# Optimization experiments

Hardware: AMD Instinct MI355X
Metric: run time of the kernel (lower is better)

## Reference

```python
import jax, jax.numpy as jnp
import numpy as np
from math import sqrt

B, NQ, SK, ISIZE, HSIZE, OSIZE, H = 4, 2048, 2048, 1024, 1024, 1024, 16
D = HSIZE // H  # attn_dim = 64
IEPS = 1e-32
NEG = -1e32

def setup_inputs() -> dict:
    key = jax.random.key(0)
    ks = jax.random.split(key, 9)
    scale = 1.0 / sqrt(ISIZE)
    return {
        "iQ": jax.random.normal(ks[0], (B, NQ, ISIZE), jnp.float32),
        "iK": jax.random.normal(ks[1], (B, SK, ISIZE), jnp.float32),
        "iV": jax.random.normal(ks[2], (B, SK, ISIZE), jnp.float32),
        "mask": jax.random.randint(ks[3], (B, NQ, SK), 0, 2).astype(bool),
        # torch nn.Linear weights: [out_features, in_features]
        "Wq": jax.random.normal(ks[4], (HSIZE, ISIZE), jnp.float32) * scale,
        "Wk": jax.random.normal(ks[5], (HSIZE, ISIZE), jnp.float32) * scale,
        "Wv": jax.random.normal(ks[6], (HSIZE, ISIZE), jnp.float32) * scale,
        "Wo": jax.random.normal(ks[7], (OSIZE, HSIZE), jnp.float32) * scale,
        "sn_bias": jnp.zeros((1,), jnp.float32),  # SparseNormer bias
    }

def reference(iQ, iK, iV, mask, Wq, Wk, Wv, Wo, sn_bias):
    b, nq, _ = iQ.shape
    sk = iK.shape[1]
    # projections, split into heads: [b, h, n, d]
    q = (iQ @ Wq.T).reshape(b, nq, H, D).transpose(0, 2, 1, 3)
    k = (iK @ Wk.T).reshape(b, sk, H, D).transpose(0, 2, 1, 3)
    v = (iV @ Wv.T).reshape(b, sk, H, D).transpose(0, 2, 1, 3)
    # scaled dot-product scores: [b, h, nq, sk]
    scores = jnp.einsum("bhqd,bhkd->bhqk", q, k) / sqrt(D)
    scores = jnp.where(mask[:, None, :, :], NEG, scores)
    # SparseNormer: relu(x + bias)^2 normalized along last dim
    t = jax.nn.relu(scores + sn_bias)
    t = t * t
    attn = t / (t.sum(-1, keepdims=True) + IEPS)
    o = jnp.einsum("bhqk,bhkd->bhqd", attn, v)
    o = o.transpose(0, 2, 1, 3).reshape(b, nq, HSIZE)
    return o @ Wo.T
```

## Files before the change

### kernel.cpp

```cpp
#include <hip/hip_runtime.h>
#include <stdint.h>

#define B_   4
#define NQ_  2048
#define SK_  2048
#define H_   16
#define HS_  1024
#define D_   64
#define TOKc ((size_t)B_ * NQ_ * HS_)
#define WEc  ((size_t)HS_ * HS_)

typedef __attribute__((ext_vector_type(8))) short bf16x8;
typedef __attribute__((ext_vector_type(4))) float f32x4;
typedef __attribute__((ext_vector_type(2))) float f32x2;
typedef __attribute__((ext_vector_type(8))) unsigned short u16x8;
typedef __attribute__((ext_vector_type(4))) int i32x4;

#define DEVI __device__ __forceinline__

DEVI unsigned short f2bf_hu(float f) {
  union { float f; unsigned int i; } x; x.f = f;
  return (unsigned short)((x.i + 0x8000u) >> 16);
}
DEVI unsigned int pack2(float a, float b) {
  union { float f; unsigned int i; } x, y; x.f = a; y.f = b;
  return __builtin_amdgcn_perm(y.i + 0x8000u, x.i + 0x8000u, 0x07060302u);
}
DEVI u16x8 cvt8(f32x4 lo, f32x4 hi) {
  union { u16x8 s; unsigned int w[4]; } r;
  r.w[0] = pack2(lo[0], lo[1]);
  r.w[1] = pack2(lo[2], lo[3]);
  r.w[2] = pack2(hi[0], hi[1]);
  r.w[3] = pack2(hi[2], hi[3]);
  return r.s;
}
DEVI void async16(void* lds, const void* g) {
  __builtin_amdgcn_global_load_lds(
      (const __attribute__((address_space(1))) unsigned int*)g,
      (__attribute__((address_space(3))) unsigned int*)lds, 16, 0, 0);
}

DEVI f32x2 pkfma(f32x2 a, f32x2 b, f32x2 c) {
  f32x2 d;
  asm("v_pk_fma_f32 %0, %1, %2, %3" : "=v"(d) : "v"(a), "v"(b), "v"(c));
  return d;
}
DEVI f32x2 pkmul(f32x2 a, f32x2 b) {
  f32x2 d;
  asm("v_pk_mul_f32 %0, %1, %2" : "=v"(d) : "v"(a), "v"(b));
  return d;
}
DEVI f32x2 pkadd(f32x2 a, f32x2 b) {
  f32x2 d;
  asm("v_pk_add_f32 %0, %1, %2" : "=v"(d) : "v"(a), "v"(b));
  return d;
}
DEVI unsigned int cvtpk_bf16(float lo, float hi) {
  unsigned int r;
  asm("v_cvt_pk_bf16_f32 %0, %1, %2" : "=v"(r) : "v"(lo), "v"(hi));
  return r;
}
template <int OFF>
DEVI float keepf(float x, unsigned int nb) {
  int k;
  asm("v_bfe_i32 %0, %1, %2, 1" : "=v"(k) : "v"(nb), "i"(OFF));
  union { float f; int i; } u; u.f = x; u.i &= k;
  return u.f;
}

#define SWZB(row, colb) ((((row) * 128) + (colb)) ^ (((row) & 7) << 4))

__global__ __launch_bounds__(256)
void cvt_prep(const float* __restrict__ a, unsigned short* __restrict__ ab,
              const float* __restrict__ wsrc, unsigned short* __restrict__ wdst,
              int naBlocks) {
  const int bi = blockIdx.x;
  const float* s; unsigned short* d; size_t base;
  if (bi < naBlocks) { s = a;    d = ab;   base = (size_t)bi * 2048; }
  else               { s = wsrc; d = wdst; base = (size_t)(bi - naBlocks) * 2048; }
  const size_t o = base + (size_t)threadIdx.x * 8;
  f32x4 lo = *(const f32x4*)(s + o);
  f32x4 hi = *(const f32x4*)(s + o + 4);
  *(u16x8*)(d + o) = cvt8(lo, hi);
}

__global__ __launch_bounds__(256)
void cvt_all(const float* __restrict__ iQ, const float* __restrict__ iK,
             const float* __restrict__ iV, const float* __restrict__ Wq,
             const float* __restrict__ Wk, const float* __restrict__ Wv,
             const float* __restrict__ Wo, unsigned short* __restrict__ ACT,
             unsigned short* __restrict__ WALL) {
  const int bi = blockIdx.x;
  const float* s; unsigned short* d; size_t base;
  if (bi < 12288) {
    const int which = bi >> 12;
    s = (which == 0) ? iQ : (which == 1) ? iK : iV;
    d = ACT + (size_t)which * TOKc;
    base = (size_t)(bi & 4095) * 2048;
  } else {
    const int wi = (bi - 12288) >> 9;
    s = (wi == 0) ? Wq : (wi == 1) ? Wk : (wi == 2) ? Wv : Wo;
    d = WALL + (size_t)wi * WEc;
    base = (size_t)((bi - 12288) & 511) * 2048;
  }
  const size_t o = base + (size_t)threadIdx.x * 8;
  f32x4 lo = *(const f32x4*)(s + o);
  f32x4 hi = *(const f32x4*)(s + o + 4);
  *(u16x8*)(d + o) = cvt8(lo, hi);
}

__global__ __launch_bounds__(256)
void pack_mask(const int* __restrict__ m, unsigned long long* __restrict__ bits) {
  const size_t tid = (size_t)blockIdx.x * 256 + threadIdx.x;
  const unsigned long long bal = __ballot(m[tid] != 0);
  if ((threadIdx.x & 63) == 0) bits[tid >> 6] = bal;
}

template <bool CF32>
DEVI void gemm_body_pipe(const unsigned short* __restrict__ A,
                         const unsigned short* __restrict__ Wb,
                         void* __restrict__ Cp, int M, int N, int K,
                         unsigned short* As, unsigned short* Bs) {
  const int t = threadIdx.x;
  const int w = t >> 6, l = t & 63;
  const int lm = l & 15, lg = l >> 4;
  const int bm = blockIdx.x * 128, bn = blockIdx.y * 128;
  const int wm = (w >> 1) * 64, wn = (w & 1) * 64;

  const int sr = t >> 2;
  const int sg = ((t & 3) ^ ((t >> 3) & 3)) * 8;
  const unsigned short* Ag0 = A + (size_t)(bm + sr) * K + sg;
  const unsigned short* Ag1 = A + (size_t)(bm + sr + 64) * K + sg;
  const unsigned short* Wg0 = Wb + (size_t)(bn + sr) * K + sg;
  const unsigned short* Wg1 = Wb + (size_t)(bn + sr + 64) * K + sg;

  const int fx = (lm >> 1) & 3;
  f32x4 acc[4][4] = {};

  auto stage = [&](int bi, int k0) {
    unsigned short* la = As + bi * 4096 + t * 8;
    unsigned short* lb = Bs + bi * 4096 + t * 8;
    async16(la,        Ag0 + k0);
    async16(la + 2048, Ag1 + k0);
    async16(lb,        Wg0 + k0);
    async16(lb + 2048, Wg1 + k0);
  };

  stage(0, 0);
  int cur = 0;
  for (int k0 = 0; k0 < K; k0 += 32) {
    if (k0 + 32 < K) {
      stage(cur ^ 1, k0 + 32);
      asm volatile("s_waitcnt vmcnt(4)" ::: "memory");
    } else {
      asm volatile("s_waitcnt vmcnt(0)" ::: "memory");
    }
    __builtin_amdgcn_sched_barrier(0);
    __builtin_amdgcn_s_barrier();
    const unsigned short* Ab = As + cur * 4096;
    const unsigned short* Bb = Bs + cur * 4096;
    bf16x8 aF[4], bF[4];
#pragma unroll
    for (int i = 0; i < 4; i++)
      aF[i] = *(const bf16x8*)&Ab[(wm + i * 16 + lm) * 32 + ((lg ^ fx) * 8)];
#pragma unroll
    for (int i = 0; i < 4; i++)
      bF[i] = *(const bf16x8*)&Bb[(wn + i * 16 + lm) * 32 + ((lg ^ fx) * 8)];
    __builtin_amdgcn_s_setprio(1);
#pragma unroll
    for (int i = 0; i < 4; i++)
#pragma unroll
      for (int j = 0; j < 4; j++)
        acc[i][j] = __builtin_amdgcn_mfma_f32_16x16x32_bf16(aF[i], bF[j], acc[i][j], 0, 0, 0);
    __builtin_amdgcn_s_setprio(0);
    __builtin_amdgcn_s_barrier();
    cur ^= 1;
  }
#pragma unroll
  for (int i = 0; i < 4; i++)
#pragma unroll
    for (int j = 0; j < 4; j++) {
      const int row = bm + wm + i * 16 + lg * 4;
      const int col = bn + wn + j * 16 + lm;
#pragma unroll
      for (int r = 0; r < 4; r++) {
        if constexpr (CF32) {
          ((float*)Cp)[(size_t)(row + r) * N + col] = acc[i][j][r];
        } else {
          ((unsigned short*)Cp)[(size_t)(row + r) * N + col] = f2bf_hu(acc[i][j][r]);
        }
      }
    }
}

template <bool CF32>
__global__ __launch_bounds__(256)
void gemm_bb(const unsigned short* __restrict__ A, const unsigned short* __restrict__ Wb,
             void* __restrict__ Cp, int M, int N, int K) {
  __shared__ unsigned short As[2 * 128 * 32];
  __shared__ unsigned short Bs[2 * 128 * 32];
  gemm_body_pipe<CF32>(A, Wb, Cp, M, N, K, As, Bs);
}

__global__ __launch_bounds__(256)
void gemm_qkv(const unsigned short* __restrict__ ACT, const unsigned short* __restrict__ WALL,
              unsigned short* __restrict__ Qb, unsigned short* __restrict__ Kb,
              unsigned short* __restrict__ Vb, int M, int N, int K) {
  __shared__ unsigned short As[2 * 128 * 32];
  __shared__ unsigned short Bs[2 * 128 * 32];
  const int z = blockIdx.z;
  const unsigned short* A = ACT + (size_t)z * (size_t)M * (size_t)K;
  const unsigned short* W = WALL + (size_t)z * (size_t)N * (size_t)K;
  unsigned short* C = (z == 0) ? Qb : ((z == 1) ? Kb : Vb);
  gemm_body_pipe<false>(A, W, (void*)C, M, N, K, As, Bs);
}

template <bool ABF16, bool CF32>
__global__ __launch_bounds__(256)
void gemm_bt(const void* __restrict__ Ap, const float* __restrict__ W,
             void* __restrict__ Cp, int M, int N, int K) {
  __shared__ unsigned short As[128 * 40];
  __shared__ unsigned short Bs[128 * 40];
  const int t = threadIdx.x;
  const int w = t >> 6, l = t & 63;
  const int lm = l & 15, lg = l >> 4;
  const int bm = blockIdx.x * 128, bn = blockIdx.y * 128;
  const int wm = (w >> 1) * 64, wn = (w & 1) * 64;
  const int sr = t >> 2, sc = (t & 3) * 8;
  const float* Af = (const float*)Ap;
  const unsigned short* Ab = (const unsigned short*)Ap;
  const size_t ao0 = (size_t)(bm + sr) * K + sc;
  const size_t ao1 = (size_t)(bm + sr + 64) * K + sc;
  const size_t wo0 = (size_t)(bn + sr) * K + sc;
  const size_t wo1 = (size_t)(bn + sr + 64) * K + sc;
  auto loadA = [&](size_t off) -> u16x8 {
    if constexpr (ABF16) {
      return *(const u16x8*)(Ab + off);
    } else {
      f32x4 lo = *(const f32x4*)(Af + off);
      f32x4 hi = *(const f32x4*)(Af + off + 4);
      return cvt8(lo, hi);
    }
  };
  auto loadW = [&](size_t off) -> u16x8 {
    f32x4 lo = *(const f32x4*)(W + off);
    f32x4 hi = *(const f32x4*)(W + off + 4);
    return cvt8(lo, hi);
  };
  u16x8 pa0 = loadA(ao0), pa1 = loadA(ao1);
  u16x8 pb0 = loadW(wo0), pb1 = loadW(wo1);
  f32x4 acc[4][4] = {};
  for (int k0 = 0; k0 < K; k0 += 32) {
    *(u16x8*)&As[sr * 40 + sc]        = pa0;
    *(u16x8*)&As[(sr + 64) * 40 + sc] = pa1;
    *(u16x8*)&Bs[sr * 40 + sc]        = pb0;
    *(u16x8*)&Bs[(sr + 64) * 40 + sc] = pb1;
    __syncthreads();
    if (k0 + 32 < K) {
      pa0 = loadA(ao0 + k0 + 32);
      pa1 = loadA(ao1 + k0 + 32);
      pb0 = loadW(wo0 + k0 + 32);
      pb1 = loadW(wo1 + k0 + 32);
    }
    bf16x8 aF[4], bF[4];
#pragma unroll
    for (int i = 0; i < 4; i++)
      aF[i] = *(const bf16x8*)&As[(wm + i * 16 + lm) * 40 + lg * 8];
#pragma unroll
    for (int i = 0; i < 4; i++)
      bF[i] = *(const bf16x8*)&Bs[(wn + i * 16 + lm) * 40 + lg * 8];
#pragma unroll
    for (int i = 0; i < 4; i++)
#pragma unroll
      for (int j = 0; j < 4; j++)
        acc[i][j] = __builtin_amdgcn_mfma_f32_16x16x32_bf16(aF[i], bF[j], acc[i][j], 0, 0, 0);
    __syncthreads();
  }
#pragma unroll
  for (int i = 0; i < 4; i++)
#pragma unroll
    for (int j = 0; j < 4; j++) {
      const int row = bm + wm + i * 16 + lg * 4;
      const int col = bn + wn + j * 16 + lm;
#pragma unroll
      for (int r = 0; r < 4; r++) {
        if constexpr (CF32) {
          ((float*)Cp)[(size_t)(row + r) * N + col] = acc[i][j][r];
        } else {
          ((unsigned short*)Cp)[(size_t)(row + r) * N + col] = f2bf_hu(acc[i][j][r]);
        }
      }
    }
}

template <int MODE>
__global__ __launch_bounds__(256)
void attn_sn(const unsigned short* __restrict__ Qb,
             const unsigned short* __restrict__ Kb,
             const unsigned short* __restrict__ Vb,
             const int* __restrict__ mask,
             const unsigned int* __restrict__ bits,
             const float* __restrict__ snb,
             unsigned short* __restrict__ Ob) {
  __shared__ unsigned short Ks[64 * 64];
  __shared__ unsigned short Vt[64 * 64];
  __shared__ unsigned short Pq[128 * 64];

  const int h = blockIdx.x, qt = blockIdx.y, b = blockIdx.z;
  const int t = threadIdx.x, w = t >> 6, l = t & 63;
  const int lm = l & 15, lg = l >> 4;
  const int q0 = qt * 128;
  const int wk = (w >> 1) * 32;
  const int wn = (w & 1) * 64;
  const float bias = snb[0];

  char* KsB = (char*)Ks;
  char* VtB = (char*)Vt;
  char* PqB = (char*)Pq;

  bf16x8 bQ[4][2];
#pragma unroll
  for (int ni = 0; ni < 4; ni++)
#pragma unroll
    for (int kf = 0; kf < 2; kf++) {
      const int qq = q0 + wn + ni * 16 + lm;
      bQ[ni][kf] = *(const bf16x8*)&Qb[(size_t)(b * NQ_ + qq) * HS_ + h * D_ + kf * 32 + lg * 8];
    }

  const int kr = t >> 3, kcb = (t & 7) * 16;
  const unsigned short* Kg = Kb + (size_t)(b * SK_) * HS_ + h * D_ + (t & 7) * 8;
  const int va = t & 31;
  const int vc = (t >> 5) * 8;
  const unsigned short* Vg = Vb + (size_t)(b * SK_) * HS_ + h * D_ + vc;
  const int* mbase = mask + (size_t)b * NQ_ * SK_;

  f32x4 oacc[2][4] = {};
  float dpart[4] = {0.f, 0.f, 0.f, 0.f};
  f32x2 dp2[4] = {};

  u16x8 pk0 = *(const u16x8*)(Kg + (size_t)(kr) * HS_);
  u16x8 pk1 = *(const u16x8*)(Kg + (size_t)(32 + kr) * HS_);
  u16x8 pv0 = *(const u16x8*)(Vg + (size_t)(2 * va) * HS_);
  u16x8 pv1 = *(const u16x8*)(Vg + (size_t)(2 * va + 1) * HS_);

  for (int kt = 0; kt < SK_ / 64; kt++) {
    const int kk0 = kt * 64;
    *(u16x8*)(KsB + SWZB(kr, kcb))      = pk0;
    *(u16x8*)(KsB + SWZB(kr + 32, kcb)) = pk1;
    {
      union { u16x8 s; unsigned int w4[4]; } a0, a1;
      a0.s = pv0; a1.s = pv1;
#pragma unroll
      for (int ww = 0; ww < 4; ww++) {
        unsigned int lo = __builtin_amdgcn_perm(a1.w4[ww], a0.w4[ww], 0x05040100u);
        unsigned int hi = __builtin_amdgcn_perm(a1.w4[ww], a0.w4[ww], 0x07060302u);
        *(unsigned int*)(VtB + SWZB(vc + 2 * ww,     4 * va)) = lo;
        *(unsigned int*)(VtB + SWZB(vc + 2 * ww + 1, 4 * va)) = hi;
      }
    }
    __syncthreads();

    if (kt + 1 < SK_ / 64) {
      const int nk0 = kk0 + 64;
      pk0 = *(const u16x8*)(Kg + (size_t)(nk0 + kr) * HS_);
      pk1 = *(const u16x8*)(Kg + (size_t)(nk0 + 32 + kr) * HS_);
      pv0 = *(const u16x8*)(Vg + (size_t)(nk0 + 2 * va) * HS_);
      pv1 = *(const u16x8*)(Vg + (size_t)(nk0 + 2 * va + 1) * HS_);
    }

    i32x4 mq[4][2];
    unsigned int mb[4];
    if constexpr (MODE == 1) {
#pragma unroll
      for (int ni = 0; ni < 4; ni++)
        mb[ni] = bits[(size_t)(b * NQ_ + q0 + wn + ni * 16 + lm) * 64 + kt * 2 + (wk >> 5)];
    } else {
#pragma unroll
      for (int ni = 0; ni < 4; ni++) {
        const int* mrow = mbase + (size_t)(q0 + wn + ni * 16 + lm) * SK_ + kk0 + wk + lg * 4;
#pragma unroll
        for (int mi = 0; mi < 2; mi++) mq[ni][mi] = *(const i32x4*)(mrow + mi * 16);
      }
    }

    bf16x8 aK[2][2];
#pragma unroll
    for (int mi = 0; mi < 2; mi++)
#pragma unroll
      for (int kf = 0; kf < 2; kf++)
        aK[mi][kf] = *(const bf16x8*)(KsB + SWZB(wk + mi * 16 + lm, kf * 64 + lg * 16));
    f32x4 sf[2][4] = {};
    __builtin_amdgcn_s_setprio(1);
#pragma unroll
    for (int mi = 0; mi < 2; mi++)
#pragma unroll
      for (int ni = 0; ni < 4; ni++) {
        sf[mi][ni] = __builtin_amdgcn_mfma_f32_16x16x32_bf16(aK[mi][0], bQ[ni][0], sf[mi][ni], 0, 0, 0);
        sf[mi][ni] = __builtin_amdgcn_mfma_f32_16x16x32_bf16(aK[mi][1], bQ[ni][1], sf[mi][ni], 0, 0, 0);
      }
    __builtin_amdgcn_s_setprio(0);

    if constexpr (MODE == 1) {
      const f32x2 c8 = {0.125f, 0.125f};
      const f32x2 bias2 = {bias, bias};
#pragma unroll
      for (int ni = 0; ni < 4; ni++) {
        const unsigned int nb = (~mb[ni]) >> (lg * 4);
#pragma unroll
        for (int mi = 0; mi < 2; mi++) {
          const f32x4 sv = sf[mi][ni];
          f32x2 t01 = pkfma((f32x2){sv[0], sv[1]}, c8, bias2);
          f32x2 t23 = pkfma((f32x2){sv[2], sv[3]}, c8, bias2);
          float x0 = fmaxf(t01[0], 0.f), x1 = fmaxf(t01[1], 0.f);
          float x2 = fmaxf(t23[0], 0.f), x3 = fmaxf(t23[1], 0.f);
          if (mi == 0) {
            x0 = keepf<0>(x0, nb);  x1 = keepf<1>(x1, nb);
            x2 = keepf<2>(x2, nb);  x3 = keepf<3>(x3, nb);
          } else {
            x0 = keepf<16>(x0, nb); x1 = keepf<17>(x1, nb);
            x2 = keepf<18>(x2, nb); x3 = keepf<19>(x3, nb);
          }
          const f32x2 u01 = pkmul((f32x2){x0, x1}, (f32x2){x0, x1});
          const f32x2 u23 = pkmul((f32x2){x2, x3}, (f32x2){x2, x3});
          dp2[ni] = pkadd(dp2[ni], u01);
          dp2[ni] = pkadd(dp2[ni], u23);
          const unsigned long long pk =
              (unsigned long long)cvtpk_bf16(u01[0], u01[1]) |
              ((unsigned long long)cvtpk_bf16(u23[0], u23[1]) << 32);
          *(unsigned long long*)(PqB + SWZB(wn + ni * 16 + lm, (wk + mi * 16 + lg * 4) * 2)) = pk;
        }
      }
    } else {
#pragma unroll
      for (int ni = 0; ni < 4; ni++) {
        float dsum = 0.f;
#pragma unroll
        for (int mi = 0; mi < 2; mi++) {
          const f32x4 sv = sf[mi][ni];
          float x2[4];
#pragma unroll
          for (int r = 0; r < 4; r++) {
            float x = fmaxf(sv[r] * 0.125f + bias, 0.f);
            x = mq[ni][mi][r] ? 0.f : x;
            x2[r] = x * x;
            dsum += x2[r];
          }
          const unsigned long long pk =
              (unsigned long long)pack2(x2[0], x2[1]) |
              ((unsigned long long)pack2(x2[2], x2[3]) << 32);
          *(unsigned long long*)(PqB + SWZB(wn + ni * 16 + lm, (wk + mi * 16 + lg * 4) * 2)) = pk;
        }
        dpart[ni] += dsum;
      }
    }
    __syncthreads();

#pragma unroll
    for (int k2 = 0; k2 < 2; k2++) {
      bf16x8 aV[2], bP[4];
#pragma unroll
      for (int mi = 0; mi < 2; mi++)
        aV[mi] = *(const bf16x8*)(VtB + SWZB(wk + mi * 16 + lm, k2 * 64 + lg * 16));
#pragma unroll
      for (int ni = 0; ni < 4; ni++)
        bP[ni] = *(const bf16x8*)(PqB + SWZB(wn + ni * 16 + lm, k2 * 64 + lg * 16));
      __builtin_amdgcn_s_setprio(1);
#pragma unroll
      for (int mi = 0; mi < 2; mi++)
#pragma unroll
        for (int ni = 0; ni < 4; ni++)
          oacc[mi][ni] = __builtin_amdgcn_mfma_f32_16x16x32_bf16(aV[mi], bP[ni], oacc[mi][ni], 0, 0, 0);
      __builtin_amdgcn_s_setprio(0);
    }
    __syncthreads();
  }

  float* denomS = (float*)Ks;
#pragma unroll
  for (int ni = 0; ni < 4; ni++) {
    float v = (MODE == 1) ? (dp2[ni][0] + dp2[ni][1]) : dpart[ni];
    v += __shfl_xor(v, 16, 64);
    v += __shfl_xor(v, 32, 64);
    dpart[ni] = v;
  }
  if (((w >> 1) == 0) && (lg == 0)) {
#pragma unroll
    for (int ni = 0; ni < 4; ni++) denomS[wn + ni * 16 + lm] = dpart[ni];
  }
  __syncthreads();
  if (((w >> 1) == 1) && (lg == 0)) {
#pragma unroll
    for (int ni = 0; ni < 4; ni++) denomS[wn + ni * 16 + lm] += dpart[ni];
  }
  __syncthreads();

#pragma unroll
  for (int ni = 0; ni < 4; ni++) {
    const int ql = wn + ni * 16 + lm;
    const float inv = 1.0f / (denomS[ql] + 1e-32f);
#pragma unroll
    for (int mi = 0; mi < 2; mi++) {
      const int d0 = wk + mi * 16 + lg * 4;
      const f32x4 ov = oacc[mi][ni];
      const unsigned long long pk =
          (unsigned long long)cvtpk_bf16(ov[0] * inv, ov[1] * inv) |
          ((unsigned long long)cvtpk_bf16(ov[2] * inv, ov[3] * inv) << 32);
      *(unsigned long long*)(PqB + SWZB(ql, d0 * 2)) = pk;
    }
  }
  __syncthreads();
  const int qf = t >> 1;
  unsigned short* orow = Ob + (size_t)(b * NQ_ + q0 + qf) * HS_ + h * D_ + (t & 1) * 32;
#pragma unroll
  for (int j = 0; j < 4; j++) {
    u16x8 vv = *(const u16x8*)(PqB + SWZB(qf, (t & 1) * 64 + j * 16));
    *(u16x8*)(orow + j * 8) = vv;
  }
}

extern "C" void kernel_launch(void* const* d_in, const int* in_sizes, int n_in,
                              void* d_out, int out_size, void* d_ws, size_t ws_size,
                              hipStream_t stream) {
  (void)in_sizes; (void)n_in; (void)out_size;
  const float* iQ  = (const float*)d_in[0];
  const float* iK  = (const float*)d_in[1];
  const float* iV  = (const float*)d_in[2];
  const int*   msk = (const int*)d_in[3];
  const float* Wq  = (const float*)d_in[4];
  const float* Wk  = (const float*)d_in[5];
  const float* Wv  = (const float*)d_in[6];
  const float* Wo  = (const float*)d_in[7];
  const float* snb = (const float*)d_in[8];
  float* out = (float*)d_out;

  const size_t TOK = TOKc;
  const size_t WE  = WEc;
  const size_t BITS_B = (size_t)B_ * NQ_ * SK_ / 8;
  const size_t NEED1 = (3 * TOK + WE) * 2 + BITS_B;
  const size_t NEEDF = (6 * TOK + 4 * WE) * 2 + BITS_B;

  const dim3 gg(64, 8, 1), bb(256, 1, 1);
  const dim3 g3(64, 8, 3);
  const dim3 ga(H_, NQ_ / 128, B_);
  const int M = B_ * NQ_, N = HS_, K = HS_;

  if (ws_size >= NEEDF) {
    unsigned short* ACT  = (unsigned short*)d_ws;
    unsigned short* WALL = ACT + 3 * TOK;
    unsigned short* Kb   = WALL + 4 * WE;
    unsigned short* Vb   = Kb + TOK;
    unsigned short* Ob   = Vb + TOK;
    unsigned int*  bits  = (unsigned int*)(Ob + TOK);
    unsigned short* Qb   = (unsigned short*)d_out;
    unsigned short* Wob  = WALL + 3 * WE;

    hipLaunchKernelGGL(cvt_all, dim3(14336), bb, 0, stream,
                       iQ, iK, iV, Wq, Wk, Wv, Wo, ACT, WALL);
    hipLaunchKernelGGL(gemm_qkv, g3, bb, 0, stream, ACT, WALL, Qb, Kb, Vb, M, N, K);
    hipLaunchKernelGGL(pack_mask, dim3(65536), bb, 0, stream,
                       msk, (unsigned long long*)bits);
    hipLaunchKernelGGL((attn_sn<1>), ga, bb, 0, stream,
                       Qb, Kb, Vb, msk, bits, snb, Ob);
    hipLaunchKernelGGL((gemm_bb<true>), gg, bb, 0, stream, Ob, Wob, (void*)out, M, N, K);
  } else if (ws_size >= NEED1) {
    unsigned short* Kb = (unsigned short*)d_ws;
    unsigned short* Vb = Kb + TOK;
    unsigned short* Ob = Vb + TOK;
    unsigned short* Wb = Ob + TOK;
    unsigned int* bits = (unsigned int*)(Wb + WE);
    unsigned short* out_us = (unsigned short*)d_out;
    unsigned short* Qb  = out_us;
    unsigned short* INb = out_us + TOK;

    hipLaunchKernelGGL(cvt_prep, dim3(4608), bb, 0, stream, iQ, INb, Wq, Wb, 4096);
    hipLaunchKernelGGL((gemm_bb<false>), gg, bb, 0, stream, INb, Wb, (void*)Qb, M, N, K);
    hipLaunchKernelGGL(cvt_prep, dim3(4608), bb, 0, stream, iK, INb, Wk, Wb, 4096);
    hipLaunchKernelGGL((gemm_bb<false>), gg, bb, 0, stream, INb, Wb, (void*)Kb, M, N, K);
    hipLaunchKernelGGL(cvt_prep, dim3(4608), bb, 0, stream, iV, INb, Wv, Wb, 4096);
    hipLaunchKernelGGL((gemm_bb<false>), gg, bb, 0, stream, INb, Wb, (void*)Vb, M, N, K);
    hipLaunchKernelGGL(cvt_prep, dim3(512), bb, 0, stream,
                       (const float*)nullptr, (unsigned short*)nullptr, Wo, Wb, 0);
    hipLaunchKernelGGL(pack_mask, dim3(65536), bb, 0, stream,
                       msk, (unsigned long long*)bits);
    hipLaunchKernelGGL((attn_sn<1>), ga, bb, 0, stream,
                       Qb, Kb, Vb, msk, bits, snb, Ob);
    hipLaunchKernelGGL((gemm_bb<true>), gg, bb, 0, stream, Ob, Wb, (void*)out, M, N, K);
  } else {
    unsigned short *Qb, *Kb, *Vb, *Ob;
    if (ws_size >= 4 * TOK * sizeof(unsigned short)) {
      Qb = (unsigned short*)d_ws;
      Kb = Qb + TOK;
      Vb = Qb + 2 * TOK;
      Ob = Qb + 3 * TOK;
    } else {
      Qb = (unsigned short*)d_out;
      Kb = (unsigned short*)d_ws;
      Vb = Kb + TOK;
      Ob = Kb + 2 * TOK;
    }
    hipLaunchKernelGGL((gemm_bt<false, false>), gg, bb, 0, stream, (const void*)iQ, Wq, (void*)Qb, M, N, K);
    hipLaunchKernelGGL((gemm_bt<false, false>), gg, bb, 0, stream, (const void*)iK, Wk, (void*)Kb, M, N, K);
    hipLaunchKernelGGL((gemm_bt<false, false>), gg, bb, 0, stream, (const void*)iV, Wv, (void*)Vb, M, N, K);
    hipLaunchKernelGGL((attn_sn<0>), ga, bb, 0, stream,
                       Qb, Kb, Vb, msk, (const unsigned int*)nullptr, snb, Ob);
    hipLaunchKernelGGL((gemm_bt<true, true>), gg, bb, 0, stream, (const void*)Ob, Wo, (void*)out, M, N, K);
  }
}
```

Baseline: 443.6 us.

## Use 256x128-tile, BK=64 GEMM kernels with 512 threads for projections

Adds a new bf16 GEMM body with 256x128 output tiles, a K-step of 64, 8 waves, and double-buffered async global-to-LDS loads with an XOR swizzle. It replaces both the fused QKV projection GEMM and the output-projection GEMM on the full-workspace path. The larger tile raises data reuse per LDS load and halves the K-loop iteration count and barrier count. In exchange it needs 96KB of LDS per block, which limits occupancy to one block per CU despite the launch bound asking for two, and it launches fewer blocks.

```diff
diff --git a/kernel.cpp b/kernel.cpp
--- a/kernel.cpp
+++ b/kernel.cpp
@@ -117,6 +117,125 @@
 }
 
 template <bool CF32>
+DEVI void gemm_big_body(const unsigned short* __restrict__ A,
+                        const unsigned short* __restrict__ W,
+                        void* __restrict__ Cp, int M, int N, int K,
+                        unsigned short* As, unsigned short* Bs) {
+  const int t = threadIdx.x;
+  const int w = t >> 6, l = t & 63;
+  const int lm = l & 15, lg = l >> 4;
+  const int bm = blockIdx.x * 256, bn = blockIdx.y * 128;
+  const int wm = (w >> 1) * 64;
+  const int wn = (w & 1) * 64;
+
+  const int srow = t >> 3;
+  const int sg = (((t & 7) ^ ((t >> 3) & 7))) * 8;
+  const unsigned short* Ag[4];
+  const unsigned short* Bg[2];
+#pragma unroll
+  for (int c = 0; c < 4; c++)
+    Ag[c] = A + (size_t)(bm + c * 64 + srow) * K + sg;
+#pragma unroll
+  for (int c = 0; c < 2; c++)
+    Bg[c] = W + (size_t)(bn + c * 64 + srow) * K + sg;
+
+  auto stage = [&](int bi, int k0) {
+    char* la = (char*)As + bi * 32768;
+    char* lb = (char*)Bs + bi * 16384;
+#pragma unroll
+    for (int c = 0; c < 4; c++) async16(la + c * 8192 + t * 16, Ag[c] + k0);
+#pragma unroll
+    for (int c = 0; c < 2; c++) async16(lb + c * 8192 + t * 16, Bg[c] + k0);
+  };
+
+  const int axor = (lm & 7) << 4;
+  f32x4 acc[4][4] = {};
+
+  stage(0, 0);
+  int cur = 0;
+  for (int k0 = 0; k0 < K; k0 += 64) {
+    if (k0 + 64 < K) {
+      stage(cur ^ 1, k0 + 64);
+      asm volatile("s_waitcnt vmcnt(6)" ::: "memory");
+    } else {
+      asm volatile("s_waitcnt vmcnt(0)" ::: "memory");
+    }
+    __builtin_amdgcn_sched_barrier(0);
+    __builtin_amdgcn_s_barrier();
+    __builtin_amdgcn_sched_barrier(0);
+
+    const char* Ab = (const char*)As + cur * 32768;
+    const char* Bb = (const char*)Bs + cur * 16384;
+    bf16x8 aF[4][2], bF[4][2];
+#pragma unroll
+    for (int mi = 0; mi < 4; mi++)
+#pragma unroll
+      for (int kk = 0; kk < 2; kk++)
+        aF[mi][kk] = *(const bf16x8*)(Ab + (wm + mi * 16 + lm) * 128 +
+                                      ((kk * 64 + lg * 16) ^ axor));
+#pragma unroll
+    for (int ni = 0; ni < 4; ni++)
+#pragma unroll
+      for (int kk = 0; kk < 2; kk++)
+        bF[ni][kk] = *(const bf16x8*)(Bb + (wn + ni * 16 + lm) * 128 +
+                                      ((kk * 64 + lg * 16) ^ axor));
+    __builtin_amdgcn_s_setprio(1);
+#pragma unroll
+    for (int kk = 0; kk < 2; kk++)
+#pragma unroll
+      for (int mi = 0; mi < 4; mi++)
+#pragma unroll
+        for (int ni = 0; ni < 4; ni++)
+          acc[mi][ni] = __builtin_amdgcn_mfma_f32_16x16x32_bf16(
+              aF[mi][kk], bF[ni][kk], acc[mi][ni], 0, 0, 0);
+    __builtin_amdgcn_s_setprio(0);
+    __builtin_amdgcn_sched_barrier(0);
+    __builtin_amdgcn_s_barrier();
+    __builtin_amdgcn_sched_barrier(0);
+    cur ^= 1;
+  }
+
+#pragma unroll
+  for (int mi = 0; mi < 4; mi++)
+#pragma unroll
+    for (int ni = 0; ni < 4; ni++) {
+      const int row = bm + wm + mi * 16 + lg * 4;
+      const int col = bn + wn + ni * 16 + lm;
+#pragma unroll
+      for (int r = 0; r < 4; r++) {
+        if constexpr (CF32) {
+          ((float*)Cp)[(size_t)(row + r) * N + col] = acc[mi][ni][r];
+        } else {
+          ((unsigned short*)Cp)[(size_t)(row + r) * N + col] = f2bf_hu(acc[mi][ni][r]);
+        }
+      }
+    }
+}
+
+template <bool CF32>
+__global__ __launch_bounds__(512, 2)
+void gemm_big(const unsigned short* __restrict__ A, const unsigned short* __restrict__ W,
+              void* __restrict__ Cp, int M, int N, int K) {
+  __shared__ unsigned short As[2 * 256 * 64];
+  __shared__ unsigned short Bs[2 * 128 * 64];
+  gemm_big_body<CF32>(A, W, Cp, M, N, K, As, Bs);
+}
+
+__global__ __launch_bounds__(512, 2)
+void gemm_qkv_big(const unsigned short* __restrict__ ACT,
+                  const unsigned short* __restrict__ WALL,
+                  unsigned short* __restrict__ Qb, unsigned short* __restrict__ Kb,
+                  unsigned short* __restrict__ Vb, int M, int N, int K) {
+  __shared__ unsigned short As[2 * 256 * 64];
+  __shared__ unsigned short Bs[2 * 128 * 64];
+  const int z = blockIdx.z;
+  const unsigned short* A = ACT + (size_t)z * (size_t)M * (size_t)K;
+  const unsigned short* W = WALL + (size_t)z * (size_t)N * (size_t)K;
+  unsigned short* C = (z == 0) ? Qb : ((z == 1) ? Kb : Vb);
+  gemm_big_body<false>(A, W, (void*)C, M, N, K, As, Bs);
+}
+
+template <bool CF32>
 DEVI void gemm_body_pipe(const unsigned short* __restrict__ A,
                          const unsigned short* __restrict__ Wb,
                          void* __restrict__ Cp, int M, int N, int K,
@@ -200,19 +319,6 @@
   __shared__ unsigned short As[2 * 128 * 32];
   __shared__ unsigned short Bs[2 * 128 * 32];
   gemm_body_pipe<CF32>(A, Wb, Cp, M, N, K, As, Bs);
-}
-
-__global__ __launch_bounds__(256)
-void gemm_qkv(const unsigned short* __restrict__ ACT, const unsigned short* __restrict__ WALL,
-              unsigned short* __restrict__ Qb, unsigned short* __restrict__ Kb,
-              unsigned short* __restrict__ Vb, int M, int N, int K) {
-  __shared__ unsigned short As[2 * 128 * 32];
-  __shared__ unsigned short Bs[2 * 128 * 32];
-  const int z = blockIdx.z;
-  const unsigned short* A = ACT + (size_t)z * (size_t)M * (size_t)K;
-  const unsigned short* W = WALL + (size_t)z * (size_t)N * (size_t)K;
-  unsigned short* C = (z == 0) ? Qb : ((z == 1) ? Kb : Vb);
-  gemm_body_pipe<false>(A, W, (void*)C, M, N, K, As, Bs);
 }
 
 template <bool ABF16, bool CF32>
@@ -540,8 +646,8 @@
   const size_t NEEDF = (6 * TOK + 4 * WE) * 2 + BITS_B;
 
   const dim3 gg(64, 8, 1), bb(256, 1, 1);
-  const dim3 g3(64, 8, 3);
   const dim3 ga(H_, NQ_ / 128, B_);
+  const dim3 gbig(32, 8, 1), gbig3(32, 8, 3), b512(512, 1, 1);
   const int M = B_ * NQ_, N = HS_, K = HS_;
 
   if (ws_size >= NEEDF) {
@@ -556,12 +662,14 @@
 
     hipLaunchKernelGGL(cvt_all, dim3(14336), bb, 0, stream,
                        iQ, iK, iV, Wq, Wk, Wv, Wo, ACT, WALL);
-    hipLaunchKernelGGL(gemm_qkv, g3, bb, 0, stream, ACT, WALL, Qb, Kb, Vb, M, N, K);
+    hipLaunchKernelGGL(gemm_qkv_big, gbig3, b512, 0, stream,
+                       ACT, WALL, Qb, Kb, Vb, M, N, K);
     hipLaunchKernelGGL(pack_mask, dim3(65536), bb, 0, stream,
                        msk, (unsigned long long*)bits);
     hipLaunchKernelGGL((attn_sn<1>), ga, bb, 0, stream,
                        Qb, Kb, Vb, msk, bits, snb, Ob);
-    hipLaunchKernelGGL((gemm_bb<true>), gg, bb, 0, stream, Ob, Wob, (void*)out, M, N, K);
+    hipLaunchKernelGGL((gemm_big<true>), gbig, b512, 0, stream,
+                       Ob, Wob, (void*)out, M, N, K);
   } else if (ws_size >= NEED1) {
     unsigned short* Kb = (unsigned short*)d_ws;
     unsigned short* Vb = Kb + TOK;
```

New measurement: 448.4 us. About the same (+1.1%).

## Add 256x256-tile 8-wave GEMM kernel for QKV and output projections

Applied to the files above, without the earlier changes.

Introduces a new bf16 GEMM with 256x256 block tiles, 512 threads (8 waves), a 64-wide K step, double-buffered 128KB LDS with an XOR swizzle, async global-to-LDS loads and a phased MFMA schedule that uses setprio. It replaces the 128x128 GEMM for the fused QKV projection and for the output projection. The larger tiles raise reuse and arithmetic intensity per LDS byte. In exchange, occupancy drops to one block per CU, and the output GEMM launches only 128 blocks, which may leave some CUs idle.

```diff
diff --git a/kernel.cpp b/kernel.cpp
--- a/kernel.cpp
+++ b/kernel.cpp
@@ -117,6 +117,185 @@
 }
 
 template <bool CF32>
+DEVI void gemm8_body(const unsigned short* __restrict__ A,
+                     const unsigned short* __restrict__ W,
+                     void* __restrict__ Cp, int M, int N, int K, char* Lds) {
+  const int t = threadIdx.x;
+  const int w = t >> 6, l = t & 63;
+  const int lm = l & 15, lg = l >> 4;
+  const int bm = blockIdx.x * 256, bn = blockIdx.y * 256;
+  const int wm = (w >> 2) * 128;
+  const int wn = (w & 3) * 64;
+
+  const int sr8 = l >> 3;
+  const int scol = ((l & 7) ^ sr8) * 8;
+  const unsigned short* gA00 = A + (size_t)(bm +       w * 16 +     sr8) * K + scol;
+  const unsigned short* gA01 = A + (size_t)(bm +       w * 16 + 8 + sr8) * K + scol;
+  const unsigned short* gA10 = A + (size_t)(bm + 128 + w * 16 +     sr8) * K + scol;
+  const unsigned short* gA11 = A + (size_t)(bm + 128 + w * 16 + 8 + sr8) * K + scol;
+  const unsigned short* gB00 = W + (size_t)(bn +       w * 16 +     sr8) * K + scol;
+  const unsigned short* gB01 = W + (size_t)(bn +       w * 16 + 8 + sr8) * K + scol;
+  const unsigned short* gB10 = W + (size_t)(bn + 128 + w * 16 +     sr8) * K + scol;
+  const unsigned short* gB11 = W + (size_t)(bn + 128 + w * 16 + 8 + sr8) * K + scol;
+  const int ldst = w * 2048 + l * 16;
+
+  auto stage2 = [&](int buf, int half, const unsigned short* g0,
+                    const unsigned short* g1, int kofs) {
+    char* p = Lds + buf * 65536 + half * 16384 + ldst;
+    async16(p,        g0 + kofs);
+    async16(p + 1024, g1 + kofs);
+  };
+
+  auto rdA = [&](int buf, int row, int ks) -> bf16x8 {
+    const char* p = Lds + buf * 65536 + (row >> 7) * 16384 + (row & 127) * 128 +
+                    ((ks * 64 + lg * 16) ^ ((row & 7) << 4));
+    return *(const bf16x8*)p;
+  };
+  auto rdB = [&](int buf, int row, int ks) -> bf16x8 {
+    const char* p = Lds + 32768 + buf * 65536 + (row >> 7) * 16384 +
+                    (row & 127) * 128 + ((ks * 64 + lg * 16) ^ ((row & 7) << 4));
+    return *(const bf16x8*)p;
+  };
+
+  f32x4 acc[8][4] = {};
+  const int NT = K >> 6;
+
+  stage2(0, 0, gA00, gA01, 0);
+  stage2(0, 1, gA10, gA11, 0);
+  stage2(0, 2, gB00, gB01, 0);
+  stage2(0, 3, gB10, gB11, 0);
+  asm volatile("s_waitcnt vmcnt(0)" ::: "memory");
+  __builtin_amdgcn_sched_barrier(0);
+  __builtin_amdgcn_s_barrier();
+
+  for (int tt = 0; tt < NT; tt++) {
+    const int cur = tt & 1, nxt = cur ^ 1;
+    const int ko = (tt + 1) * 64;
+    const bool pre = (tt + 1 < NT);
+    bf16x8 aF[4][2], bF0[2][2], bF1[2][2];
+
+#pragma unroll
+    for (int mf = 0; mf < 4; mf++)
+#pragma unroll
+      for (int ks = 0; ks < 2; ks++)
+        aF[mf][ks] = rdA(cur, wm + mf * 16 + lm, ks);
+#pragma unroll
+    for (int nf = 0; nf < 2; nf++)
+#pragma unroll
+      for (int ks = 0; ks < 2; ks++)
+        bF0[nf][ks] = rdB(cur, wn + nf * 16 + lm, ks);
+    if (pre) { stage2(nxt, 0, gA00, gA01, ko); stage2(nxt, 1, gA10, gA11, ko); }
+    __builtin_amdgcn_s_barrier();
+    asm volatile("s_waitcnt lgkmcnt(0)" ::: "memory");
+    __builtin_amdgcn_sched_barrier(0);
+    __builtin_amdgcn_s_setprio(1);
+#pragma unroll
+    for (int ks = 0; ks < 2; ks++)
+#pragma unroll
+      for (int mf = 0; mf < 4; mf++)
+#pragma unroll
+        for (int nf = 0; nf < 2; nf++)
+          acc[mf][nf] = __builtin_amdgcn_mfma_f32_16x16x32_bf16(
+              aF[mf][ks], bF0[nf][ks], acc[mf][nf], 0, 0, 0);
+    __builtin_amdgcn_s_setprio(0);
+    __builtin_amdgcn_s_barrier();
+
+#pragma unroll
+    for (int nf = 0; nf < 2; nf++)
+#pragma unroll
+      for (int ks = 0; ks < 2; ks++)
+        bF1[nf][ks] = rdB(cur, wn + (nf + 2) * 16 + lm, ks);
+    if (pre) { stage2(nxt, 2, gB00, gB01, ko); stage2(nxt, 3, gB10, gB11, ko); }
+    __builtin_amdgcn_s_barrier();
+    asm volatile("s_waitcnt lgkmcnt(0)" ::: "memory");
+    __builtin_amdgcn_sched_barrier(0);
+    __builtin_amdgcn_s_setprio(1);
+#pragma unroll
+    for (int ks = 0; ks < 2; ks++)
+#pragma unroll
+      for (int mf = 0; mf < 4; mf++)
+#pragma unroll
+        for (int nf = 0; nf < 2; nf++)
+          acc[mf][nf + 2] = __builtin_amdgcn_mfma_f32_16x16x32_bf16(
+              aF[mf][ks], bF1[nf][ks], acc[mf][nf + 2], 0, 0, 0);
+    __builtin_amdgcn_s_setprio(0);
+    __builtin_amdgcn_s_barrier();
+
+#pragma unroll
+    for (int mf = 0; mf < 4; mf++)
+#pragma unroll
+      for (int ks = 0; ks < 2; ks++)
+        aF[mf][ks] = rdA(cur, wm + (mf + 4) * 16 + lm, ks);
+    __builtin_amdgcn_s_barrier();
+    asm volatile("s_waitcnt lgkmcnt(0)" ::: "memory");
+    __builtin_amdgcn_sched_barrier(0);
+    __builtin_amdgcn_s_setprio(1);
+#pragma unroll
+    for (int ks = 0; ks < 2; ks++)
+#pragma unroll
+      for (int mf = 0; mf < 4; mf++)
+#pragma unroll
+        for (int nf = 0; nf < 2; nf++)
+          acc[mf + 4][nf + 2] = __builtin_amdgcn_mfma_f32_16x16x32_bf16(
+              aF[mf][ks], bF1[nf][ks], acc[mf + 4][nf + 2], 0, 0, 0);
+    __builtin_amdgcn_s_setprio(0);
+    __builtin_amdgcn_s_barrier();
+
+    __builtin_amdgcn_s_setprio(1);
+#pragma unroll
+    for (int ks = 0; ks < 2; ks++)
+#pragma unroll
+      for (int mf = 0; mf < 4; mf++)
+#pragma unroll
+        for (int nf = 0; nf < 2; nf++)
+          acc[mf + 4][nf] = __builtin_amdgcn_mfma_f32_16x16x32_bf16(
+              aF[mf][ks], bF0[nf][ks], acc[mf + 4][nf], 0, 0, 0);
+    __builtin_amdgcn_s_setprio(0);
+
+    asm volatile("s_waitcnt vmcnt(0)" ::: "memory");
+    __builtin_amdgcn_sched_barrier(0);
+    __builtin_amdgcn_s_barrier();
+  }
+
+#pragma unroll
+  for (int mf = 0; mf < 8; mf++)
+#pragma unroll
+    for (int nf = 0; nf < 4; nf++) {
+      const int row = bm + wm + mf * 16 + lg * 4;
+      const int col = bn + wn + nf * 16 + lm;
+#pragma unroll
+      for (int r = 0; r < 4; r++) {
+        if constexpr (CF32) {
+          ((float*)Cp)[(size_t)(row + r) * N + col] = acc[mf][nf][r];
+        } else {
+          ((unsigned short*)Cp)[(size_t)(row + r) * N + col] = f2bf_hu(acc[mf][nf][r]);
+        }
+      }
+    }
+}
+
+template <bool CF32>
+__global__ __launch_bounds__(512)
+void gemm8(const unsigned short* __restrict__ A, const unsigned short* __restrict__ W,
+           void* __restrict__ Cp, int M, int N, int K) {
+  __shared__ __align__(16) char Lds[131072];
+  gemm8_body<CF32>(A, W, Cp, M, N, K, Lds);
+}
+
+__global__ __launch_bounds__(512)
+void gemm8_qkv(const unsigned short* __restrict__ ACT,
+               const unsigned short* __restrict__ WALL,
+               unsigned short* __restrict__ Qb, unsigned short* __restrict__ Kb,
+               unsigned short* __restrict__ Vb, int M, int N, int K) {
+  __shared__ __align__(16) char Lds[131072];
+  const int z = blockIdx.z;
+  const unsigned short* A = ACT + (size_t)z * (size_t)M * (size_t)K;
+  const unsigned short* W = WALL + (size_t)z * (size_t)N * (size_t)K;
+  unsigned short* C = (z == 0) ? Qb : ((z == 1) ? Kb : Vb);
+  gemm8_body<false>(A, W, (void*)C, M, N, K, Lds);
+}
+
+template <bool CF32>
 DEVI void gemm_body_pipe(const unsigned short* __restrict__ A,
                          const unsigned short* __restrict__ Wb,
                          void* __restrict__ Cp, int M, int N, int K,
@@ -200,19 +379,6 @@
   __shared__ unsigned short As[2 * 128 * 32];
   __shared__ unsigned short Bs[2 * 128 * 32];
   gemm_body_pipe<CF32>(A, Wb, Cp, M, N, K, As, Bs);
-}
-
-__global__ __launch_bounds__(256)
-void gemm_qkv(const unsigned short* __restrict__ ACT, const unsigned short* __restrict__ WALL,
-              unsigned short* __restrict__ Qb, unsigned short* __restrict__ Kb,
-              unsigned short* __restrict__ Vb, int M, int N, int K) {
-  __shared__ unsigned short As[2 * 128 * 32];
-  __shared__ unsigned short Bs[2 * 128 * 32];
-  const int z = blockIdx.z;
-  const unsigned short* A = ACT + (size_t)z * (size_t)M * (size_t)K;
-  const unsigned short* W = WALL + (size_t)z * (size_t)N * (size_t)K;
-  unsigned short* C = (z == 0) ? Qb : ((z == 1) ? Kb : Vb);
-  gemm_body_pipe<false>(A, W, (void*)C, M, N, K, As, Bs);
 }
 
 template <bool ABF16, bool CF32>
@@ -540,8 +706,8 @@
   const size_t NEEDF = (6 * TOK + 4 * WE) * 2 + BITS_B;
 
   const dim3 gg(64, 8, 1), bb(256, 1, 1);
-  const dim3 g3(64, 8, 3);
   const dim3 ga(H_, NQ_ / 128, B_);
+  const dim3 g8(32, 4, 1), g83(32, 4, 3), b512(512, 1, 1);
   const int M = B_ * NQ_, N = HS_, K = HS_;
 
   if (ws_size >= NEEDF) {
@@ -556,12 +722,14 @@
 
     hipLaunchKernelGGL(cvt_all, dim3(14336), bb, 0, stream,
                        iQ, iK, iV, Wq, Wk, Wv, Wo, ACT, WALL);
-    hipLaunchKernelGGL(gemm_qkv, g3, bb, 0, stream, ACT, WALL, Qb, Kb, Vb, M, N, K);
+    hipLaunchKernelGGL(gemm8_qkv, g83, b512, 0, stream,
+                       ACT, WALL, Qb, Kb, Vb, M, N, K);
     hipLaunchKernelGGL(pack_mask, dim3(65536), bb, 0, stream,
                        msk, (unsigned long long*)bits);
     hipLaunchKernelGGL((attn_sn<1>), ga, bb, 0, stream,
                        Qb, Kb, Vb, msk, bits, snb, Ob);
-    hipLaunchKernelGGL((gemm_bb<true>), gg, bb, 0, stream, Ob, Wob, (void*)out, M, N, K);
+    hipLaunchKernelGGL((gemm8<true>), g8, b512, 0, stream,
+                       Ob, Wob, (void*)out, M, N, K);
   } else if (ws_size >= NEED1) {
     unsigned short* Kb = (unsigned short*)d_ws;
     unsigned short* Vb = Kb + TOK;
```

Result: no change. 447.9 us (+1.0%).
